# Optimization experiments

Measured on AMD Instinct MI355X. Metric: run time of the kernel, lower is better.

## Reference

```python
import jax, jax.numpy as jnp
import numpy as np

EMBED, HEADS, FF, WIN = 512, 8, 2048, 64
SIGMA, PSTRENGTH, PERIOD, THRESH = 2.0, 1.0, 100.0, 0.0


def layer_norm(x, g, b, eps=1e-5):
    mu = jnp.mean(x, axis=-1, keepdims=True)
    var = jnp.var(x, axis=-1, keepdims=True)
    return (x - mu) * jax.lax.rsqrt(var + eps) * g + b


def setup_inputs() -> dict:
    key = jax.random.key(0)
    ks = jax.random.split(key, 16)
    s = 1.0 / np.sqrt(EMBED)
    sf = 1.0 / np.sqrt(FF)
    inp = {
        "src": jax.random.normal(ks[0], (8, 2048, EMBED), dtype=jnp.float32),
        "Wq": jax.random.normal(ks[1], (EMBED, EMBED), dtype=jnp.float32) * s,
        "bq": jnp.zeros((EMBED,), jnp.float32),
        "Wk": jax.random.normal(ks[2], (EMBED, EMBED), dtype=jnp.float32) * s,
        "bk": jnp.zeros((EMBED,), jnp.float32),
        "Wv": jax.random.normal(ks[3], (EMBED, EMBED), dtype=jnp.float32) * s,
        "bv": jnp.zeros((EMBED,), jnp.float32),
        "Wo": jax.random.normal(ks[4], (EMBED, EMBED), dtype=jnp.float32) * s,
        "bo": jnp.zeros((EMBED,), jnp.float32),
        "Wg": jax.random.normal(ks[5], (EMBED, 1), dtype=jnp.float32) * s,
        "bg": jnp.zeros((1,), jnp.float32),
        "W1": jax.random.normal(ks[6], (EMBED, FF), dtype=jnp.float32) * s,
        "b1": jnp.zeros((FF,), jnp.float32),
        "W2": jax.random.normal(ks[7], (FF, EMBED), dtype=jnp.float32) * sf,
        "b2": jnp.zeros((EMBED,), jnp.float32),
        "ln1_g": jnp.ones((EMBED,), jnp.float32),
        "ln1_b": jnp.zeros((EMBED,), jnp.float32),
        "ln2_g": jnp.ones((EMBED,), jnp.float32),
        "ln2_b": jnp.zeros((EMBED,), jnp.float32),
    }
    return inp


def gated_sparse_attn(x, Wq, bq, Wk, bk, Wv, bv, Wo, bo, Wg, bg):
    B, S, D = x.shape
    H, dh = HEADS, D // HEADS
    q = (x @ Wq + bq).reshape(B, S, H, dh).transpose(0, 2, 1, 3)  # [B,H,S,dh]
    k = (x @ Wk + bk).reshape(B, S, H, dh).transpose(0, 2, 1, 3)
    v = (x @ Wv + bv).reshape(B, S, H, dh).transpose(0, 2, 1, 3)
    scores = jnp.einsum('bhqd,bhkd->bhqk', q, k) / jnp.sqrt(jnp.float32(dh))
    idx = jnp.arange(S, dtype=jnp.float32)
    dist = idx[:, None] - idx[None, :]  # [S,S]
    gauss_bias = jnp.exp(-(dist * dist) / (2.0 * SIGMA * SIGMA))
    per_bias = PSTRENGTH * jnp.cos(2.0 * jnp.pi * dist / PERIOD)
    scores = scores + gauss_bias + per_bias  # positional biases baked into scores
    local = jnp.abs(dist) <= WIN  # local-window sparsity mask
    scores = jnp.where(local, scores, jnp.float32(-1e9))
    attn = jax.nn.softmax(scores, axis=-1)
    out = jnp.einsum('bhqk,bhkd->bhqd', attn, v)
    out = out.transpose(0, 2, 1, 3).reshape(B, S, D) @ Wo + bo
    gate = jax.nn.sigmoid(x @ Wg + bg)  # [B,S,1] learned gating
    gate = jnp.where(gate > THRESH, gate, jnp.float32(0.0))
    return gate * out


def reference(src, Wq, bq, Wk, bk, Wv, bv, Wo, bo, Wg, bg, W1, b1, W2, b2, ln1_g, ln1_b, ln2_g, ln2_b):
    # dropout is identity in eval mode
    attn_out = gated_sparse_attn(src, Wq, bq, Wk, bk, Wv, bv, Wo, bo, Wg, bg)
    x = layer_norm(src + attn_out, ln1_g, ln1_b)
    ff = jax.nn.relu(x @ W1 + b1) @ W2 + b2
    return layer_norm(x + ff, ln2_g, ln2_b)
```

## Files before the change

kernel.cpp:

```cpp
#include <hip/hip_runtime.h>
#include <hip/hip_bf16.h>
#include <math.h>

#define S_LEN   2048
#define D_MOD   512
#define N_HEADS 8
#define D_HEAD  64
#define FF_DIM  2048
#define M_ROWS  16384
#define BHSD    8388608

typedef __attribute__((ext_vector_type(8))) __bf16 bf16x8;
typedef __attribute__((ext_vector_type(4))) float  f32x4;
typedef unsigned short u16;

__device__ __forceinline__ u16 f2bf(float f) {
  unsigned u = __float_as_uint(f);
  u += 0x7fffu + ((u >> 16) & 1u);
  return (u16)(u >> 16);
}
__device__ __forceinline__ float bf2f(u16 h) { return __uint_as_float(((unsigned)h) << 16); }

__device__ __forceinline__ f32x4 mfma16(bf16x8 a, bf16x8 b, f32x4 c) {
  return __builtin_amdgcn_mfma_f32_16x16x32_bf16(a, b, c, 0, 0, 0);
}

__device__ __forceinline__ void async16(void* lds, const void* g) {
  __builtin_amdgcn_global_load_lds(
      (const __attribute__((address_space(1))) unsigned int*)g,
      (__attribute__((address_space(3))) unsigned int*)lds, 16, 0, 0);
}

#define BAR()    asm volatile("s_barrier" ::: "memory")
#define WAITV(n) asm volatile("s_waitcnt vmcnt(" #n ")" ::: "memory")
#define WAITL()  asm volatile("s_waitcnt lgkmcnt(0)" ::: "memory")

__device__ __forceinline__ int swz384(int row, int bir) {
  return row * 384 + ((bir & ~127) | ((bir ^ ((row & 7) << 4)) & 127));
}

__global__ __launch_bounds__(256) void cvt_gate(const float* __restrict__ src,
                                                const float* __restrict__ Wg,
                                                const float* __restrict__ bg,
                                                u16* __restrict__ xb,
                                                float* __restrict__ gate) {
  const int wid = threadIdx.x >> 6, lane = threadIdx.x & 63;
  const size_t row = (size_t)blockIdx.x * 4 + wid;
  const float4* s = reinterpret_cast<const float4*>(src + row * D_MOD);
  const float4* w = reinterpret_cast<const float4*>(Wg);
  float4 a0 = s[lane * 2], a1 = s[lane * 2 + 1];
  float4 w0 = w[lane * 2], w1 = w[lane * 2 + 1];
  float acc = a0.x * w0.x + a0.y * w0.y + a0.z * w0.z + a0.w * w0.w +
              a1.x * w1.x + a1.y * w1.y + a1.z * w1.z + a1.w * w1.w;
#pragma unroll
  for (int m = 1; m < 64; m <<= 1) acc += __shfl_xor(acc, m);
  ushort4 h0, h1;
  h0.x = f2bf(a0.x); h0.y = f2bf(a0.y); h0.z = f2bf(a0.z); h0.w = f2bf(a0.w);
  h1.x = f2bf(a1.x); h1.y = f2bf(a1.y); h1.z = f2bf(a1.z); h1.w = f2bf(a1.w);
  ushort4* ob = reinterpret_cast<ushort4*>(xb + row * D_MOD);
  ob[lane * 2] = h0; ob[lane * 2 + 1] = h1;
  if (lane == 0) {
    float g = 1.f / (1.f + __expf(-(acc + bg[0])));
    gate[row] = g > 0.f ? g : 0.f;
  }
}

__global__ void transpose_cvt(const float* __restrict__ in, u16* __restrict__ out,
                              int K, int N) {
  __shared__ float t[32][33];
  const int n0 = blockIdx.x * 32, k0 = blockIdx.y * 32;
  const int tx = threadIdx.x, ty = threadIdx.y;
#pragma unroll
  for (int i = 0; i < 4; ++i)
    t[ty + 8 * i][tx] = in[(size_t)(k0 + ty + 8 * i) * N + n0 + tx];
  __syncthreads();
#pragma unroll
  for (int i = 0; i < 4; ++i)
    out[(size_t)(n0 + ty + 8 * i) * K + k0 + tx] = f2bf(t[tx][ty + 8 * i]);
}

__global__ __launch_bounds__(256) void ln1red_k(const float* __restrict__ src,
                                                const float* __restrict__ gate,
                                                const u16* __restrict__ p0,
                                                const u16* __restrict__ p1,
                                                const float* __restrict__ bo,
                                                const float* __restrict__ gam,
                                                const float* __restrict__ bet,
                                                u16* __restrict__ outb) {
  const int wid = threadIdx.x >> 6, lane = threadIdx.x & 63;
  const size_t row = (size_t)blockIdx.x * 4 + wid;
  const size_t base = row * D_MOD;
  const float g = gate[row];
  const float4*  sp = reinterpret_cast<const float4*>(src + base);
  const ushort4* a  = reinterpret_cast<const ushort4*>(p0 + base);
  const ushort4* c  = reinterpret_cast<const ushort4*>(p1 + base);
  const float4*  bb = reinterpret_cast<const float4*>(bo);
  float4 s0 = sp[lane * 2], s1 = sp[lane * 2 + 1];
  ushort4 a0 = a[lane * 2], a1 = a[lane * 2 + 1];
  ushort4 c0 = c[lane * 2], c1 = c[lane * 2 + 1];
  float4 d0 = bb[lane * 2], d1 = bb[lane * 2 + 1];
  float4 v0, v1;
  v0.x = s0.x + g * (bf2f(a0.x) + bf2f(c0.x) + d0.x);
  v0.y = s0.y + g * (bf2f(a0.y) + bf2f(c0.y) + d0.y);
  v0.z = s0.z + g * (bf2f(a0.z) + bf2f(c0.z) + d0.z);
  v0.w = s0.w + g * (bf2f(a0.w) + bf2f(c0.w) + d0.w);
  v1.x = s1.x + g * (bf2f(a1.x) + bf2f(c1.x) + d1.x);
  v1.y = s1.y + g * (bf2f(a1.y) + bf2f(c1.y) + d1.y);
  v1.z = s1.z + g * (bf2f(a1.z) + bf2f(c1.z) + d1.z);
  v1.w = s1.w + g * (bf2f(a1.w) + bf2f(c1.w) + d1.w);
  float s  = v0.x + v0.y + v0.z + v0.w + v1.x + v1.y + v1.z + v1.w;
  float s2 = v0.x * v0.x + v0.y * v0.y + v0.z * v0.z + v0.w * v0.w +
             v1.x * v1.x + v1.y * v1.y + v1.z * v1.z + v1.w * v1.w;
#pragma unroll
  for (int m = 1; m < 64; m <<= 1) { s += __shfl_xor(s, m); s2 += __shfl_xor(s2, m); }
  const float mu = s * (1.0f / 512.0f);
  const float var = s2 * (1.0f / 512.0f) - mu * mu;
  const float rs = 1.0f / sqrtf(var + 1e-5f);
  const float4* gp = reinterpret_cast<const float4*>(gam);
  const float4* bp = reinterpret_cast<const float4*>(bet);
  float4 g0 = gp[lane * 2], g1 = gp[lane * 2 + 1];
  float4 e0 = bp[lane * 2], e1 = bp[lane * 2 + 1];
  ushort4 h0, h1;
  h0.x = f2bf((v0.x - mu) * rs * g0.x + e0.x);  h0.y = f2bf((v0.y - mu) * rs * g0.y + e0.y);
  h0.z = f2bf((v0.z - mu) * rs * g0.z + e0.z);  h0.w = f2bf((v0.w - mu) * rs * g0.w + e0.w);
  h1.x = f2bf((v1.x - mu) * rs * g1.x + e1.x);  h1.y = f2bf((v1.y - mu) * rs * g1.y + e1.y);
  h1.z = f2bf((v1.z - mu) * rs * g1.z + e1.z);  h1.w = f2bf((v1.w - mu) * rs * g1.w + e1.w);
  ushort4* ob = reinterpret_cast<ushort4*>(outb + base);
  ob[lane * 2] = h0; ob[lane * 2 + 1] = h1;
}

__global__ __launch_bounds__(256) void ln2red_k(const u16* __restrict__ xb,
                                                const u16* __restrict__ p0,
                                                const u16* __restrict__ p1,
                                                const float* __restrict__ b2,
                                                const float* __restrict__ gam,
                                                const float* __restrict__ bet,
                                                float* __restrict__ out) {
  const int wid = threadIdx.x >> 6, lane = threadIdx.x & 63;
  const size_t row = (size_t)blockIdx.x * 4 + wid;
  const size_t base = row * D_MOD;
  const ushort4* xp = reinterpret_cast<const ushort4*>(xb + base);
  const ushort4* q0 = reinterpret_cast<const ushort4*>(p0 + base);
  const ushort4* q1 = reinterpret_cast<const ushort4*>(p1 + base);
  const float4* bb = reinterpret_cast<const float4*>(b2);
  ushort4 h0 = xp[lane * 2], h1 = xp[lane * 2 + 1];
  ushort4 a0 = q0[lane * 2], a1 = q0[lane * 2 + 1];
  ushort4 c0 = q1[lane * 2], c1 = q1[lane * 2 + 1];
  float4 d0 = bb[lane * 2], d1 = bb[lane * 2 + 1];
  float4 v0, v1;
  v0.x = bf2f(h0.x) + bf2f(a0.x) + bf2f(c0.x) + d0.x;
  v0.y = bf2f(h0.y) + bf2f(a0.y) + bf2f(c0.y) + d0.y;
  v0.z = bf2f(h0.z) + bf2f(a0.z) + bf2f(c0.z) + d0.z;
  v0.w = bf2f(h0.w) + bf2f(a0.w) + bf2f(c0.w) + d0.w;
  v1.x = bf2f(h1.x) + bf2f(a1.x) + bf2f(c1.x) + d1.x;
  v1.y = bf2f(h1.y) + bf2f(a1.y) + bf2f(c1.y) + d1.y;
  v1.z = bf2f(h1.z) + bf2f(a1.z) + bf2f(c1.z) + d1.z;
  v1.w = bf2f(h1.w) + bf2f(a1.w) + bf2f(c1.w) + d1.w;
  float s  = v0.x + v0.y + v0.z + v0.w + v1.x + v1.y + v1.z + v1.w;
  float s2 = v0.x * v0.x + v0.y * v0.y + v0.z * v0.z + v0.w * v0.w +
             v1.x * v1.x + v1.y * v1.y + v1.z * v1.z + v1.w * v1.w;
#pragma unroll
  for (int m = 1; m < 64; m <<= 1) { s += __shfl_xor(s, m); s2 += __shfl_xor(s2, m); }
  const float mu = s * (1.0f / 512.0f);
  const float var = s2 * (1.0f / 512.0f) - mu * mu;
  const float rs = 1.0f / sqrtf(var + 1e-5f);
  const float4* gp = reinterpret_cast<const float4*>(gam);
  const float4* bp = reinterpret_cast<const float4*>(bet);
  float4 g0 = gp[lane * 2], g1 = gp[lane * 2 + 1];
  float4 e0 = bp[lane * 2], e1 = bp[lane * 2 + 1];
  float4 o0, o1;
  o0.x = (v0.x - mu) * rs * g0.x + e0.x;  o0.y = (v0.y - mu) * rs * g0.y + e0.y;
  o0.z = (v0.z - mu) * rs * g0.z + e0.z;  o0.w = (v0.w - mu) * rs * g0.w + e0.w;
  o1.x = (v1.x - mu) * rs * g1.x + e1.x;  o1.y = (v1.y - mu) * rs * g1.y + e1.y;
  o1.z = (v1.z - mu) * rs * g1.z + e1.z;  o1.w = (v1.w - mu) * rs * g1.w + e1.w;
  float4* q = reinterpret_cast<float4*>(out + base);
  q[lane * 2] = o0; q[lane * 2 + 1] = o1;
}

struct EpiArgs {
  const float* b0; const float* b1; const float* b2;
  float* outf; u16* outb; u16* outb2;
};

template<int EPI, int LD, int NT, int KSLICE, int GX, int GY>
__device__ __forceinline__ void gemm256_body(const u16* __restrict__ A,
                                             const u16* __restrict__ Bt, EpiArgs e) {
  extern __shared__ char smem[];
  char* Asb = smem;
  char* Bsb = smem + 65536;
  const int tid = threadIdx.x;
  const int wid = tid >> 6, lane = tid & 63;
  const int sub = lane >> 4, lc = lane & 15;
  const int wr = wid >> 2, wcn = wid & 3;

  const int nwg = (int)(gridDim.x * gridDim.y * gridDim.z);
  const int orig = ((int)blockIdx.z * (int)gridDim.y + (int)blockIdx.y) * (int)gridDim.x + (int)blockIdx.x;
  const int cpx = nwg >> 3;
  const int wg = (orig & 7) * cpx + (orig >> 3);
  const int bx = wg % GX;
  const int by = (wg / GX) % GY;
  const int bz = wg / (GX * GY);
  const int m0 = by * 256, n0 = bx * 256;
  const int kb = KSLICE * bz;

  const u16* Ab = A + (size_t)m0 * LD;
  const u16* Bb = Bt + (size_t)n0 * LD;

  f32x4 acc[8][4];
#pragma unroll
  for (int i = 0; i < 8; ++i)
#pragma unroll
    for (int j = 0; j < 4; ++j) acc[i][j] = (f32x4){0.f, 0.f, 0.f, 0.f};

  const int lr0 = tid >> 3;
  const int sl  = tid & 7;

#define STAGE(BASE, SRC, BUF, KT)                                              \
  {                                                                            \
    const int kk_ = kb + (KT) * 64;                                            \
    _Pragma("unroll")                                                          \
    for (int r_ = 0; r_ < 4; ++r_) {                                           \
      const int lr_ = r_ * 64 + lr0;                                           \
      async16((BASE) + (BUF) * 32768 + r_ * 8192 + wid * 1024,                 \
              (SRC) + (size_t)lr_ * LD + kk_ + ((sl ^ (lr_ & 7)) << 3));       \
    }                                                                          \
  }
#define LDFRAG(BASE, ROW, KS) \
  (*reinterpret_cast<const bf16x8*>((BASE) + (ROW) * 128 + ((((KS) * 64) + sub * 16) ^ (((ROW) & 7) << 4))))

  STAGE(Bsb, Bb, 0, 0);
  STAGE(Asb, Ab, 0, 0);
  STAGE(Bsb, Bb, 1, 1);
  STAGE(Asb, Ab, 1, 1);
  WAITV(8);
  BAR();

  for (int t = 0; t < NT; ++t) {
    const int buf = t & 1;
    char* Abl = Asb + buf * 32768;
    char* Bbl = Bsb + buf * 32768;
    bf16x8 af[4][2], bfr[2][2][2];
#pragma unroll
    for (int f = 0; f < 4; ++f) {
      const int row = wr * 128 + f * 16 + lc;
#pragma unroll
      for (int ks = 0; ks < 2; ++ks) af[f][ks] = LDFRAG(Abl, row, ks);
    }
#pragma unroll
    for (int f = 0; f < 2; ++f) {
      const int row = wcn * 64 + f * 16 + lc;
#pragma unroll
      for (int ks = 0; ks < 2; ++ks) bfr[0][f][ks] = LDFRAG(Bbl, row, ks);
    }
    __builtin_amdgcn_s_setprio(1);
#pragma unroll
    for (int f = 0; f < 4; ++f)
#pragma unroll
      for (int c = 0; c < 2; ++c)
#pragma unroll
        for (int ks = 0; ks < 2; ++ks)
          acc[f][c] = mfma16(af[f][ks], bfr[0][c][ks], acc[f][c]);
    __builtin_amdgcn_s_setprio(0);
    BAR();
#pragma unroll
    for (int f = 0; f < 2; ++f) {
      const int row = wcn * 64 + 32 + f * 16 + lc;
#pragma unroll
      for (int ks = 0; ks < 2; ++ks) bfr[1][f][ks] = LDFRAG(Bbl, row, ks);
    }
    __builtin_amdgcn_s_setprio(1);
#pragma unroll
    for (int f = 0; f < 4; ++f)
#pragma unroll
      for (int c = 0; c < 2; ++c)
#pragma unroll
        for (int ks = 0; ks < 2; ++ks)
          acc[f][2 + c] = mfma16(af[f][ks], bfr[1][c][ks], acc[f][2 + c]);
    __builtin_amdgcn_s_setprio(0);
    WAITL();
    BAR();
    if (t + 2 < NT) STAGE(Bsb, Bb, buf, t + 2);
#pragma unroll
    for (int f = 0; f < 4; ++f) {
      const int row = wr * 128 + 64 + f * 16 + lc;
#pragma unroll
      for (int ks = 0; ks < 2; ++ks) af[f][ks] = LDFRAG(Abl, row, ks);
    }
    __builtin_amdgcn_s_setprio(1);
#pragma unroll
    for (int f = 0; f < 4; ++f)
#pragma unroll
      for (int c = 0; c < 2; ++c)
#pragma unroll
        for (int ks = 0; ks < 2; ++ks)
          acc[4 + f][2 + c] = mfma16(af[f][ks], bfr[1][c][ks], acc[4 + f][2 + c]);
    __builtin_amdgcn_s_setprio(0);
    WAITL();
    BAR();
    if (t + 2 < NT) STAGE(Asb, Ab, buf, t + 2);
    __builtin_amdgcn_s_setprio(1);
#pragma unroll
    for (int f = 0; f < 4; ++f)
#pragma unroll
      for (int c = 0; c < 2; ++c)
#pragma unroll
        for (int ks = 0; ks < 2; ++ks)
          acc[4 + f][c] = mfma16(af[f][ks], bfr[0][c][ks], acc[4 + f][c]);
    __builtin_amdgcn_s_setprio(0);
    if (t + 1 < NT) {
      if (t + 2 < NT) { WAITV(8); } else { WAITV(0); }
      BAR();
    }
  }
#undef STAGE
#undef LDFRAG

#pragma unroll
  for (int fr = 0; fr < 8; ++fr) {
    const int row0 = m0 + wr * 128 + fr * 16 + sub * 4;
#pragma unroll
    for (int fc = 0; fc < 4; ++fc) {
      const int col = n0 + wcn * 64 + fc * 16 + lc;
      f32x4 v = acc[fr][fc];
#pragma unroll
      for (int i = 0; i < 4; ++i) {
        const int row = row0 + i;
        const float val = v[i];
        if constexpr (EPI == 0) {
          const int which = col >> 9, nn = col & 511;
          const int hh = nn >> 6, dd = nn & 63;
          const float* bp = (which == 0) ? e.b0 : (which == 1) ? e.b1 : e.b2;
          const int bb = row >> 11, ss = row & 2047;
          e.outb[(size_t)which * BHSD + (((size_t)bb * N_HEADS + hh) * S_LEN + ss) * D_HEAD + dd]
              = f2bf(val + bp[nn]);
        } else if constexpr (EPI == 2) {
          float o = val + e.b0[col];
          e.outb[(size_t)row * FF_DIM + col] = f2bf(o > 0.f ? o : 0.f);
        } else {
          u16* dst = (bz == 0) ? e.outb : e.outb2;
          dst[(size_t)row * D_MOD + col] = f2bf(val);
        }
      }
    }
  }
}

__global__ __launch_bounds__(512, 2) void k_qkv(const u16* __restrict__ A, const u16* __restrict__ B, EpiArgs e) {
  gemm256_body<0, 512, 8, 0, 6, 64>(A, B, e);
}
__global__ __launch_bounds__(512, 2) void k_ff1(const u16* __restrict__ A, const u16* __restrict__ B, EpiArgs e) {
  gemm256_body<2, 512, 8, 0, 8, 64>(A, B, e);
}
__global__ __launch_bounds__(512, 2) void k_ff2(const u16* __restrict__ A, const u16* __restrict__ B, EpiArgs e) {
  gemm256_body<4, 2048, 16, 1024, 2, 64>(A, B, e);
}
__global__ __launch_bounds__(512, 2) void k_proj(const u16* __restrict__ A, const u16* __restrict__ B, EpiArgs e) {
  gemm256_body<4, 512, 4, 256, 2, 64>(A, B, e);
}

__global__ __launch_bounds__(256)
void attn_k(const u16* __restrict__ Q, const u16* __restrict__ Kt,
            const u16* __restrict__ V, u16* __restrict__ Oflat) {
  __shared__ __align__(16) u16 VT[64 * 192];
  __shared__ __align__(16) u16 P [64 * 192];
  __shared__ float tab[256];
  const int tid = threadIdx.x;
  const int wid = tid >> 6, lane = tid & 63;
  const int sub = lane >> 4, lc = lane & 15;
  const int qb = blockIdx.x, bh = blockIdx.y;
  const int bb = bh >> 3, hh = bh & 7;
  const int q0 = qb * 64, kstart = q0 - 64;
  const u16* Qb = Q  + (size_t)bh * S_LEN * D_HEAD;
  const u16* Kb = Kt + (size_t)bh * S_LEN * D_HEAD;
  const u16* Vb = V  + (size_t)bh * S_LEN * D_HEAD;

  if (tid < 255) {
    const int di = tid - 127;
    const float fd = (float)di;
    tab[tid] = (di >= -64 && di <= 64)
        ? __expf(-fd * fd * 0.125f) + __cosf(0.06283185307179586f * fd)
        : -1e9f;
  }

#pragma unroll
  for (int i = 0; i < 6; ++i) {
    const int c = tid + 256 * i;
    const int kk = c >> 3, dc = (c & 7) * 8;
    const int kg = kstart + kk;
    uint4 val = {0u, 0u, 0u, 0u};
    if (kg >= 0 && kg < S_LEN)
      val = *reinterpret_cast<const uint4*>(Vb + (size_t)kg * D_HEAD + dc);
    const u16* pv = reinterpret_cast<const u16*>(&val);
#pragma unroll
    for (int j = 0; j < 8; ++j)
      *reinterpret_cast<u16*>(reinterpret_cast<char*>(VT) + swz384(dc + j, kk * 2)) = pv[j];
  }

  bf16x8 qf[2];
#pragma unroll
  for (int ks = 0; ks < 2; ++ks)
    qf[ks] = *reinterpret_cast<const bf16x8*>(Qb + (size_t)(q0 + wid * 16 + lc) * D_HEAD + ks * 32 + sub * 8);

  f32x4 sc[12];
#pragma unroll
  for (int t = 0; t < 12; ++t) sc[t] = (f32x4){0.f, 0.f, 0.f, 0.f};
#pragma unroll
  for (int ks = 0; ks < 2; ++ks)
#pragma unroll
    for (int t = 0; t < 12; ++t) {
      int kg = kstart + t * 16 + lc;
      int kc = kg < 0 ? 0 : (kg > S_LEN - 1 ? S_LEN - 1 : kg);
      bf16x8 kf = *reinterpret_cast<const bf16x8*>(Kb + (size_t)kc * D_HEAD + ks * 32 + sub * 8);
      sc[t] = mfma16(qf[ks], kf, sc[t]);
    }
  __syncthreads();

  float rmax[4] = {-3e38f, -3e38f, -3e38f, -3e38f};
#pragma unroll
  for (int t = 0; t < 12; ++t) {
    const int kk = t * 16 + lc;
    const int kg = kstart + kk;
    const bool valid = (kg >= 0) && (kg < S_LEN);
#pragma unroll
    for (int r = 0; r < 4; ++r) {
      const int qrow = wid * 16 + sub * 4 + r;
      const float bias = valid ? tab[qrow - kk + 191] : -1e9f;
      const float sv = sc[t][r] * 0.125f + bias;
      sc[t][r] = sv;
      rmax[r] = fmaxf(rmax[r], sv);
    }
  }
#pragma unroll
  for (int m = 1; m < 16; m <<= 1)
#pragma unroll
    for (int r = 0; r < 4; ++r) rmax[r] = fmaxf(rmax[r], __shfl_xor(rmax[r], m));
  float rsum[4] = {0.f, 0.f, 0.f, 0.f};
#pragma unroll
  for (int t = 0; t < 12; ++t)
#pragma unroll
    for (int r = 0; r < 4; ++r) {
      const float p = __expf(sc[t][r] - rmax[r]);
      sc[t][r] = p; rsum[r] += p;
    }
#pragma unroll
  for (int m = 1; m < 16; m <<= 1)
#pragma unroll
    for (int r = 0; r < 4; ++r) rsum[r] += __shfl_xor(rsum[r], m);
  float rinv[4];
#pragma unroll
  for (int r = 0; r < 4; ++r) rinv[r] = 1.0f / rsum[r];
#pragma unroll
  for (int t = 0; t < 12; ++t)
#pragma unroll
    for (int r = 0; r < 4; ++r) {
      const int qrow = wid * 16 + sub * 4 + r;
      *reinterpret_cast<u16*>(reinterpret_cast<char*>(P) + swz384(qrow, (t * 16 + lc) * 2))
          = f2bf(sc[t][r] * rinv[r]);
    }
  __syncthreads();

  f32x4 oacc[4];
#pragma unroll
  for (int t = 0; t < 4; ++t) oacc[t] = (f32x4){0.f, 0.f, 0.f, 0.f};
  const int arow = wid * 16 + lc;
#pragma unroll
  for (int ks = 0; ks < 6; ++ks) {
    const int bir = ks * 64 + sub * 16;
    bf16x8 pa = *reinterpret_cast<const bf16x8*>(reinterpret_cast<char*>(P) + swz384(arow, bir));
#pragma unroll
    for (int t = 0; t < 4; ++t) {
      bf16x8 vb = *reinterpret_cast<const bf16x8*>(reinterpret_cast<char*>(VT) + swz384(t * 16 + lc, bir));
      oacc[t] = mfma16(pa, vb, oacc[t]);
    }
  }

  const size_t obase = ((size_t)bb * S_LEN + q0) * D_MOD + hh * D_HEAD;
#pragma unroll
  for (int t = 0; t < 4; ++t)
#pragma unroll
    for (int r = 0; r < 4; ++r) {
      const int qrow = wid * 16 + sub * 4 + r;
      Oflat[obase + (size_t)qrow * D_MOD + t * 16 + lc] = f2bf(oacc[t][r]);
    }
}

extern "C" void kernel_launch(void* const* d_in, const int* in_sizes, int n_in,
                              void* d_out, int out_size, void* d_ws, size_t ws_size,
                              hipStream_t stream) {
  (void)in_sizes; (void)n_in; (void)out_size; (void)ws_size;
  const float* src  = (const float*)d_in[0];
  const float* Wq   = (const float*)d_in[1];
  const float* bq   = (const float*)d_in[2];
  const float* Wk   = (const float*)d_in[3];
  const float* bk   = (const float*)d_in[4];
  const float* Wv   = (const float*)d_in[5];
  const float* bv   = (const float*)d_in[6];
  const float* Wo   = (const float*)d_in[7];
  const float* bo   = (const float*)d_in[8];
  const float* Wg   = (const float*)d_in[9];
  const float* bg   = (const float*)d_in[10];
  const float* W1   = (const float*)d_in[11];
  const float* b1   = (const float*)d_in[12];
  const float* W2   = (const float*)d_in[13];
  const float* b2   = (const float*)d_in[14];
  const float* ln1g = (const float*)d_in[15];
  const float* ln1b = (const float*)d_in[16];
  const float* ln2g = (const float*)d_in[17];
  const float* ln2b = (const float*)d_in[18];
  float* out = (float*)d_out;

  char* ws = (char*)d_ws;
  u16*   WqkvT  = (u16*)  (ws + 0);
  u16*   WoT    = (u16*)  (ws + 1572864);
  u16*   W1T    = (u16*)  (ws + 2097152);
  u16*   W2T    = (u16*)  (ws + 4194304);
  float* gatef  = (float*)(ws + 6291456);
  u16*   Xbf    = (u16*)  (ws + 6356992);
  u16*   QKVbf  = (u16*)  (ws + 23134208);
  u16*   attnfl = (u16*)  (ws + 73465856);
  u16*   pr0    = (u16*)  (ws + 90243072);
  u16*   pr1    = (u16*)  (ws + 107020288);
  u16*   xbf2   = (u16*)  (ws + 123797504);
  u16*   hbuf   = Xbf;
  u16*   pf0    = pr0;
  u16*   pf1    = pr1;

  (void)hipFuncSetAttribute((const void*)k_qkv,  hipFuncAttributeMaxDynamicSharedMemorySize, 131072);
  (void)hipFuncSetAttribute((const void*)k_ff1,  hipFuncAttributeMaxDynamicSharedMemorySize, 131072);
  (void)hipFuncSetAttribute((const void*)k_ff2,  hipFuncAttributeMaxDynamicSharedMemorySize, 131072);
  (void)hipFuncSetAttribute((const void*)k_proj, hipFuncAttributeMaxDynamicSharedMemorySize, 131072);

  dim3 tb(32, 8);
  cvt_gate<<<4096, 256, 0, stream>>>(src, Wg, bg, Xbf, gatef);
  transpose_cvt<<<dim3(16, 16), tb, 0, stream>>>(Wq, WqkvT,             512, 512);
  transpose_cvt<<<dim3(16, 16), tb, 0, stream>>>(Wk, WqkvT + 512 * 512, 512, 512);
  transpose_cvt<<<dim3(16, 16), tb, 0, stream>>>(Wv, WqkvT + 2 * 512 * 512, 512, 512);
  transpose_cvt<<<dim3(16, 16), tb, 0, stream>>>(Wo, WoT, 512, 512);
  transpose_cvt<<<dim3(64, 16), tb, 0, stream>>>(W1, W1T, 512, 2048);
  transpose_cvt<<<dim3(16, 64), tb, 0, stream>>>(W2, W2T, 2048, 512);

  EpiArgs e1{bq, bk, bv, nullptr, QKVbf, nullptr};
  k_qkv<<<dim3(6, 64, 1), 512, 131072, stream>>>(Xbf, WqkvT, e1);

  attn_k<<<dim3(32, 64), 256, 0, stream>>>(QKVbf, QKVbf + BHSD, QKVbf + 2 * BHSD, attnfl);

  EpiArgs e2{nullptr, nullptr, nullptr, nullptr, pr0, pr1};
  k_proj<<<dim3(2, 64, 2), 512, 131072, stream>>>(attnfl, WoT, e2);

  ln1red_k<<<4096, 256, 0, stream>>>(src, gatef, pr0, pr1, bo, ln1g, ln1b, xbf2);

  EpiArgs e3{b1, nullptr, nullptr, nullptr, hbuf, nullptr};
  k_ff1<<<dim3(8, 64, 1), 512, 131072, stream>>>(xbf2, W1T, e3);

  EpiArgs e4{nullptr, nullptr, nullptr, nullptr, pf0, pf1};
  k_ff2<<<dim3(2, 64, 2), 512, 131072, stream>>>(hbuf, W2T, e4);

  ln2red_k<<<4096, 256, 0, stream>>>(xbf2, pf0, pf1, b2, ln2g, ln2b, out);
}
```

Before: 222.6 us.

## Keep attention probabilities in registers via transposed MFMA and shuffles; bf16 residual in LN1

The attention kernel swaps the MFMA operand order so each lane holds one query row's scores. Softmax then needs only two cross-lane shuffles, and the normalized probabilities are packed with v_cvt_pk_bf16_f32 and rearranged by lane shuffles straight into the PV MFMA operand. This drops the P LDS round trip and one barrier. The output is staged through a small swizzled LDS buffer so each lane writes 16-byte coalesced global stores. Separately, the LN1 residual now reads the bf16 copy of src instead of fp32, which halves that read but loses precision in the residual path.

```diff
diff --git a/kernel.cpp b/kernel.cpp
--- a/kernel.cpp
+++ b/kernel.cpp
@@ -23,6 +23,12 @@
 
 __device__ __forceinline__ f32x4 mfma16(bf16x8 a, bf16x8 b, f32x4 c) {
   return __builtin_amdgcn_mfma_f32_16x16x32_bf16(a, b, c, 0, 0, 0);
+}
+
+__device__ __forceinline__ unsigned pkbf(float a, float b) {
+  unsigned r;
+  asm("v_cvt_pk_bf16_f32 %0, %1, %2" : "=v"(r) : "v"(a), "v"(b));
+  return r;
 }
 
 __device__ __forceinline__ void async16(void* lds, const void* g) {
@@ -79,7 +85,7 @@
     out[(size_t)(n0 + ty + 8 * i) * K + k0 + tx] = f2bf(t[tx][ty + 8 * i]);
 }
 
-__global__ __launch_bounds__(256) void ln1red_k(const float* __restrict__ src,
+__global__ __launch_bounds__(256) void ln1red_k(const u16* __restrict__ xb,
                                                 const float* __restrict__ gate,
                                                 const u16* __restrict__ p0,
                                                 const u16* __restrict__ p1,
@@ -91,23 +97,23 @@
   const size_t row = (size_t)blockIdx.x * 4 + wid;
   const size_t base = row * D_MOD;
   const float g = gate[row];
-  const float4*  sp = reinterpret_cast<const float4*>(src + base);
+  const ushort4* sp = reinterpret_cast<const ushort4*>(xb + base);
   const ushort4* a  = reinterpret_cast<const ushort4*>(p0 + base);
   const ushort4* c  = reinterpret_cast<const ushort4*>(p1 + base);
   const float4*  bb = reinterpret_cast<const float4*>(bo);
-  float4 s0 = sp[lane * 2], s1 = sp[lane * 2 + 1];
+  ushort4 s0 = sp[lane * 2], s1 = sp[lane * 2 + 1];
   ushort4 a0 = a[lane * 2], a1 = a[lane * 2 + 1];
   ushort4 c0 = c[lane * 2], c1 = c[lane * 2 + 1];
   float4 d0 = bb[lane * 2], d1 = bb[lane * 2 + 1];
   float4 v0, v1;
-  v0.x = s0.x + g * (bf2f(a0.x) + bf2f(c0.x) + d0.x);
-  v0.y = s0.y + g * (bf2f(a0.y) + bf2f(c0.y) + d0.y);
-  v0.z = s0.z + g * (bf2f(a0.z) + bf2f(c0.z) + d0.z);
-  v0.w = s0.w + g * (bf2f(a0.w) + bf2f(c0.w) + d0.w);
-  v1.x = s1.x + g * (bf2f(a1.x) + bf2f(c1.x) + d1.x);
-  v1.y = s1.y + g * (bf2f(a1.y) + bf2f(c1.y) + d1.y);
-  v1.z = s1.z + g * (bf2f(a1.z) + bf2f(c1.z) + d1.z);
-  v1.w = s1.w + g * (bf2f(a1.w) + bf2f(c1.w) + d1.w);
+  v0.x = bf2f(s0.x) + g * (bf2f(a0.x) + bf2f(c0.x) + d0.x);
+  v0.y = bf2f(s0.y) + g * (bf2f(a0.y) + bf2f(c0.y) + d0.y);
+  v0.z = bf2f(s0.z) + g * (bf2f(a0.z) + bf2f(c0.z) + d0.z);
+  v0.w = bf2f(s0.w) + g * (bf2f(a0.w) + bf2f(c0.w) + d0.w);
+  v1.x = bf2f(s1.x) + g * (bf2f(a1.x) + bf2f(c1.x) + d1.x);
+  v1.y = bf2f(s1.y) + g * (bf2f(a1.y) + bf2f(c1.y) + d1.y);
+  v1.z = bf2f(s1.z) + g * (bf2f(a1.z) + bf2f(c1.z) + d1.z);
+  v1.w = bf2f(s1.w) + g * (bf2f(a1.w) + bf2f(c1.w) + d1.w);
   float s  = v0.x + v0.y + v0.z + v0.w + v1.x + v1.y + v1.z + v1.w;
   float s2 = v0.x * v0.x + v0.y * v0.y + v0.z * v0.z + v0.w * v0.w +
              v1.x * v1.x + v1.y * v1.y + v1.z * v1.z + v1.w * v1.w;
@@ -362,7 +368,7 @@
 void attn_k(const u16* __restrict__ Q, const u16* __restrict__ Kt,
             const u16* __restrict__ V, u16* __restrict__ Oflat) {
   __shared__ __align__(16) u16 VT[64 * 192];
-  __shared__ __align__(16) u16 P [64 * 192];
+  __shared__ __align__(16) char Ob[8192];
   __shared__ float tab[256];
   const int tid = threadIdx.x;
   const int wid = tid >> 6, lane = tid & 63;
@@ -411,77 +417,88 @@
       int kg = kstart + t * 16 + lc;
       int kc = kg < 0 ? 0 : (kg > S_LEN - 1 ? S_LEN - 1 : kg);
       bf16x8 kf = *reinterpret_cast<const bf16x8*>(Kb + (size_t)kc * D_HEAD + ks * 32 + sub * 8);
-      sc[t] = mfma16(qf[ks], kf, sc[t]);
+      sc[t] = mfma16(kf, qf[ks], sc[t]);
     }
   __syncthreads();
 
-  float rmax[4] = {-3e38f, -3e38f, -3e38f, -3e38f};
-#pragma unroll
-  for (int t = 0; t < 12; ++t) {
-    const int kk = t * 16 + lc;
-    const int kg = kstart + kk;
-    const bool valid = (kg >= 0) && (kg < S_LEN);
+  const int qrow = wid * 16 + lc;
+  float m = -3e38f;
+#pragma unroll
+  for (int t = 0; t < 12; ++t)
 #pragma unroll
     for (int r = 0; r < 4; ++r) {
-      const int qrow = wid * 16 + sub * 4 + r;
+      const int kk = t * 16 + 4 * sub + r;
+      const int kg = kstart + kk;
+      const bool valid = (kg >= 0) && (kg < S_LEN);
       const float bias = valid ? tab[qrow - kk + 191] : -1e9f;
       const float sv = sc[t][r] * 0.125f + bias;
       sc[t][r] = sv;
-      rmax[r] = fmaxf(rmax[r], sv);
-    }
-  }
-#pragma unroll
-  for (int m = 1; m < 16; m <<= 1)
-#pragma unroll
-    for (int r = 0; r < 4; ++r) rmax[r] = fmaxf(rmax[r], __shfl_xor(rmax[r], m));
-  float rsum[4] = {0.f, 0.f, 0.f, 0.f};
+      m = fmaxf(m, sv);
+    }
+  m = fmaxf(m, __shfl_xor(m, 16));
+  m = fmaxf(m, __shfl_xor(m, 32));
+  float sum = 0.f;
 #pragma unroll
   for (int t = 0; t < 12; ++t)
 #pragma unroll
     for (int r = 0; r < 4; ++r) {
-      const float p = __expf(sc[t][r] - rmax[r]);
-      sc[t][r] = p; rsum[r] += p;
-    }
-#pragma unroll
-  for (int m = 1; m < 16; m <<= 1)
-#pragma unroll
-    for (int r = 0; r < 4; ++r) rsum[r] += __shfl_xor(rsum[r], m);
-  float rinv[4];
-#pragma unroll
-  for (int r = 0; r < 4; ++r) rinv[r] = 1.0f / rsum[r];
-#pragma unroll
-  for (int t = 0; t < 12; ++t)
-#pragma unroll
-    for (int r = 0; r < 4; ++r) {
-      const int qrow = wid * 16 + sub * 4 + r;
-      *reinterpret_cast<u16*>(reinterpret_cast<char*>(P) + swz384(qrow, (t * 16 + lc) * 2))
-          = f2bf(sc[t][r] * rinv[r]);
-    }
+      const float p = __expf(sc[t][r] - m);
+      sc[t][r] = p; sum += p;
+    }
+  sum += __shfl_xor(sum, 16);
+  sum += __shfl_xor(sum, 32);
+  const float rinv = 1.0f / sum;
+
+  f32x4 oacc[4];
+#pragma unroll
+  for (int t = 0; t < 4; ++t) oacc[t] = (f32x4){0.f, 0.f, 0.f, 0.f};
+  const int srcA = lc + ((sub & 1) << 5);
+#pragma unroll
+  for (int s = 0; s < 6; ++s) {
+    const unsigned d00 = pkbf(sc[2 * s][0] * rinv, sc[2 * s][1] * rinv);
+    const unsigned d01 = pkbf(sc[2 * s][2] * rinv, sc[2 * s][3] * rinv);
+    const unsigned d10 = pkbf(sc[2 * s + 1][0] * rinv, sc[2 * s + 1][1] * rinv);
+    const unsigned d11 = pkbf(sc[2 * s + 1][2] * rinv, sc[2 * s + 1][3] * rinv);
+    const unsigned uA0 = (unsigned)__shfl((int)d00, srcA);
+    const unsigned uA1 = (unsigned)__shfl((int)d01, srcA);
+    const unsigned uB0 = (unsigned)__shfl((int)d00, srcA + 16);
+    const unsigned uB1 = (unsigned)__shfl((int)d01, srcA + 16);
+    const unsigned vA0 = (unsigned)__shfl((int)d10, srcA);
+    const unsigned vA1 = (unsigned)__shfl((int)d11, srcA);
+    const unsigned vB0 = (unsigned)__shfl((int)d10, srcA + 16);
+    const unsigned vB1 = (unsigned)__shfl((int)d11, srcA + 16);
+    const bool lo = (sub < 2);
+    uint4 wv;
+    wv.x = lo ? uA0 : vA0;  wv.y = lo ? uA1 : vA1;
+    wv.z = lo ? uB0 : vB0;  wv.w = lo ? uB1 : vB1;
+    const bf16x8 pf = __builtin_bit_cast(bf16x8, wv);
+#pragma unroll
+    for (int t = 0; t < 4; ++t) {
+      bf16x8 vf = *reinterpret_cast<const bf16x8*>(
+          reinterpret_cast<char*>(VT) + swz384(16 * t + lc, 64 * s + 16 * sub));
+      oacc[t] = mfma16(vf, pf, oacc[t]);
+    }
+  }
+
+  char* obw = Ob + wid * 2048 + lc * 128;
+#pragma unroll
+  for (int t = 0; t < 4; ++t) {
+    const unsigned o01 = pkbf(oacc[t][0], oacc[t][1]);
+    const unsigned o23 = pkbf(oacc[t][2], oacc[t][3]);
+    const int b0 = (32 * t + 8 * sub) ^ ((lc & 7) << 4);
+    *reinterpret_cast<unsigned*>(obw + b0) = o01;
+    *reinterpret_cast<unsigned*>(obw + b0 + 4) = o23;
+  }
   __syncthreads();
-
-  f32x4 oacc[4];
-#pragma unroll
-  for (int t = 0; t < 4; ++t) oacc[t] = (f32x4){0.f, 0.f, 0.f, 0.f};
-  const int arow = wid * 16 + lc;
-#pragma unroll
-  for (int ks = 0; ks < 6; ++ks) {
-    const int bir = ks * 64 + sub * 16;
-    bf16x8 pa = *reinterpret_cast<const bf16x8*>(reinterpret_cast<char*>(P) + swz384(arow, bir));
-#pragma unroll
-    for (int t = 0; t < 4; ++t) {
-      bf16x8 vb = *reinterpret_cast<const bf16x8*>(reinterpret_cast<char*>(VT) + swz384(t * 16 + lc, bir));
-      oacc[t] = mfma16(pa, vb, oacc[t]);
-    }
-  }
-
-  const size_t obase = ((size_t)bb * S_LEN + q0) * D_MOD + hh * D_HEAD;
-#pragma unroll
-  for (int t = 0; t < 4; ++t)
-#pragma unroll
-    for (int r = 0; r < 4; ++r) {
-      const int qrow = wid * 16 + sub * 4 + r;
-      Oflat[obase + (size_t)qrow * D_MOD + t * 16 + lc] = f2bf(oacc[t][r]);
-    }
+  const int qp = lane >> 2;
+  const int cb = (lane & 3) * 32;
+  const size_t orow = (size_t)bb * S_LEN + q0 + wid * 16 + qp;
+#pragma unroll
+  for (int h = 0; h < 2; ++h) {
+    const int rb = (cb + h * 16) ^ ((qp & 7) << 4);
+    uint4 v = *reinterpret_cast<const uint4*>(Ob + wid * 2048 + qp * 128 + rb);
+    *reinterpret_cast<uint4*>(Oflat + orow * D_MOD + hh * D_HEAD + (lane & 3) * 16 + h * 8) = v;
+  }
 }
 
 extern "C" void kernel_launch(void* const* d_in, const int* in_sizes, int n_in,
@@ -547,7 +564,7 @@
   EpiArgs e2{nullptr, nullptr, nullptr, nullptr, pr0, pr1};
   k_proj<<<dim3(2, 64, 2), 512, 131072, stream>>>(attnfl, WoT, e2);
 
-  ln1red_k<<<4096, 256, 0, stream>>>(src, gatef, pr0, pr1, bo, ln1g, ln1b, xbf2);
+  ln1red_k<<<4096, 256, 0, stream>>>(Xbf, gatef, pr0, pr1, bo, ln1g, ln1b, xbf2);
 
   EpiArgs e3{b1, nullptr, nullptr, nullptr, hbuf, nullptr};
   k_ff1<<<dim3(8, 64, 1), 512, 131072, stream>>>(xbf2, W1T, e3);
```

Measured after the change: 227.0 us. No clear change (+2.0%).

## Pre-transpose V into global layout and read bf16 residual in LN1

Applied to the files above, without the earlier changes.

Adds a separate kernel that transposes V per head into a [D_HEAD, S] global buffer. The attention kernel can then fill its swizzled VT shared tile with 16-byte async copies instead of scattering 2-byte stores. The LN1 kernel also reads the residual from the bf16 copy of src instead of the fp32 original, which halves that read but lowers the residual to bf16 precision. The trade-off is an extra launch and roughly 33 MB of extra global traffic for the transposed V, and the clamped sb index at sequence edges may load shifted data where the old code zero-filled.

```diff
diff --git a/kernel.cpp b/kernel.cpp
--- a/kernel.cpp
+++ b/kernel.cpp
@@ -79,7 +79,43 @@
     out[(size_t)(n0 + ty + 8 * i) * K + k0 + tx] = f2bf(t[tx][ty + 8 * i]);
 }
 
-__global__ __launch_bounds__(256) void ln1red_k(const float* __restrict__ src,
+__global__ __launch_bounds__(256) void vtr_k(const u16* __restrict__ V,
+                                             u16* __restrict__ VT) {
+  __shared__ __align__(16) u16 T[64 * 64];
+  const int tid = threadIdx.x;
+  const int wid = tid >> 6, lane = tid & 63;
+  const int bh = blockIdx.y;
+  const int s0 = blockIdx.x * 64;
+  const u16* Vb = V + ((size_t)bh * S_LEN + s0) * D_HEAD;
+#pragma unroll
+  for (int r = 0; r < 2; ++r) {
+    const int c = r * 256 + tid;
+    const int s = c >> 3;
+    const int blk = (c & 7) ^ ((s >> 3) & 7);
+    async16((char*)T + (r * 4 + wid) * 1024, Vb + (size_t)s * D_HEAD + blk * 8);
+  }
+  __syncthreads();
+  u16* VTb = VT + (size_t)bh * D_HEAD * S_LEN;
+#pragma unroll
+  for (int r = 0; r < 2; ++r) {
+    const int d  = (r * 4 + wid) * 8 + (lane >> 3);
+    const int s8 = lane & 7;
+    ushort4 w0, w1;
+    u16 tmp[8];
+#pragma unroll
+    for (int j = 0; j < 8; ++j) {
+      const int s = s8 * 8 + j;
+      tmp[j] = *reinterpret_cast<const u16*>(
+          (const char*)T + s * 128 + ((2 * d) ^ (((s >> 3) & 7) << 4)));
+    }
+    w0.x = tmp[0]; w0.y = tmp[1]; w0.z = tmp[2]; w0.w = tmp[3];
+    w1.x = tmp[4]; w1.y = tmp[5]; w1.z = tmp[6]; w1.w = tmp[7];
+    ushort4* dst = reinterpret_cast<ushort4*>(VTb + (size_t)d * S_LEN + s0 + s8 * 8);
+    dst[0] = w0; dst[1] = w1;
+  }
+}
+
+__global__ __launch_bounds__(256) void ln1red_k(const u16* __restrict__ xb,
                                                 const float* __restrict__ gate,
                                                 const u16* __restrict__ p0,
                                                 const u16* __restrict__ p1,
@@ -91,23 +127,23 @@
   const size_t row = (size_t)blockIdx.x * 4 + wid;
   const size_t base = row * D_MOD;
   const float g = gate[row];
-  const float4*  sp = reinterpret_cast<const float4*>(src + base);
+  const ushort4* sp = reinterpret_cast<const ushort4*>(xb + base);
   const ushort4* a  = reinterpret_cast<const ushort4*>(p0 + base);
   const ushort4* c  = reinterpret_cast<const ushort4*>(p1 + base);
   const float4*  bb = reinterpret_cast<const float4*>(bo);
-  float4 s0 = sp[lane * 2], s1 = sp[lane * 2 + 1];
+  ushort4 s0 = sp[lane * 2], s1 = sp[lane * 2 + 1];
   ushort4 a0 = a[lane * 2], a1 = a[lane * 2 + 1];
   ushort4 c0 = c[lane * 2], c1 = c[lane * 2 + 1];
   float4 d0 = bb[lane * 2], d1 = bb[lane * 2 + 1];
   float4 v0, v1;
-  v0.x = s0.x + g * (bf2f(a0.x) + bf2f(c0.x) + d0.x);
-  v0.y = s0.y + g * (bf2f(a0.y) + bf2f(c0.y) + d0.y);
-  v0.z = s0.z + g * (bf2f(a0.z) + bf2f(c0.z) + d0.z);
-  v0.w = s0.w + g * (bf2f(a0.w) + bf2f(c0.w) + d0.w);
-  v1.x = s1.x + g * (bf2f(a1.x) + bf2f(c1.x) + d1.x);
-  v1.y = s1.y + g * (bf2f(a1.y) + bf2f(c1.y) + d1.y);
-  v1.z = s1.z + g * (bf2f(a1.z) + bf2f(c1.z) + d1.z);
-  v1.w = s1.w + g * (bf2f(a1.w) + bf2f(c1.w) + d1.w);
+  v0.x = bf2f(s0.x) + g * (bf2f(a0.x) + bf2f(c0.x) + d0.x);
+  v0.y = bf2f(s0.y) + g * (bf2f(a0.y) + bf2f(c0.y) + d0.y);
+  v0.z = bf2f(s0.z) + g * (bf2f(a0.z) + bf2f(c0.z) + d0.z);
+  v0.w = bf2f(s0.w) + g * (bf2f(a0.w) + bf2f(c0.w) + d0.w);
+  v1.x = bf2f(s1.x) + g * (bf2f(a1.x) + bf2f(c1.x) + d1.x);
+  v1.y = bf2f(s1.y) + g * (bf2f(a1.y) + bf2f(c1.y) + d1.y);
+  v1.z = bf2f(s1.z) + g * (bf2f(a1.z) + bf2f(c1.z) + d1.z);
+  v1.w = bf2f(s1.w) + g * (bf2f(a1.w) + bf2f(c1.w) + d1.w);
   float s  = v0.x + v0.y + v0.z + v0.w + v1.x + v1.y + v1.z + v1.w;
   float s2 = v0.x * v0.x + v0.y * v0.y + v0.z * v0.z + v0.w * v0.w +
              v1.x * v1.x + v1.y * v1.y + v1.z * v1.z + v1.w * v1.w;
@@ -360,7 +396,7 @@
 
 __global__ __launch_bounds__(256)
 void attn_k(const u16* __restrict__ Q, const u16* __restrict__ Kt,
-            const u16* __restrict__ V, u16* __restrict__ Oflat) {
+            const u16* __restrict__ VTg, u16* __restrict__ Oflat) {
   __shared__ __align__(16) u16 VT[64 * 192];
   __shared__ __align__(16) u16 P [64 * 192];
   __shared__ float tab[256];
@@ -372,7 +408,18 @@
   const int q0 = qb * 64, kstart = q0 - 64;
   const u16* Qb = Q  + (size_t)bh * S_LEN * D_HEAD;
   const u16* Kb = Kt + (size_t)bh * S_LEN * D_HEAD;
-  const u16* Vb = V  + (size_t)bh * S_LEN * D_HEAD;
+  const u16* Vtb = VTg + (size_t)bh * D_HEAD * S_LEN;
+
+#pragma unroll
+  for (int it = 0; it < 6; ++it) {
+    const int c = (wid * 6 + it) * 64 + lane;
+    const int row = c / 24;
+    const int bir = (c % 24) * 16;
+    const int swz = (bir & ~127) | ((bir ^ ((row & 7) << 4)) & 127);
+    int sb = kstart + (swz >> 1);
+    sb = sb < 0 ? 0 : (sb > S_LEN - 8 ? S_LEN - 8 : sb);
+    async16((char*)VT + (wid * 6 + it) * 1024, Vtb + (size_t)row * S_LEN + sb);
+  }
 
   if (tid < 255) {
     const int di = tid - 127;
@@ -380,20 +427,6 @@
     tab[tid] = (di >= -64 && di <= 64)
         ? __expf(-fd * fd * 0.125f) + __cosf(0.06283185307179586f * fd)
         : -1e9f;
-  }
-
-#pragma unroll
-  for (int i = 0; i < 6; ++i) {
-    const int c = tid + 256 * i;
-    const int kk = c >> 3, dc = (c & 7) * 8;
-    const int kg = kstart + kk;
-    uint4 val = {0u, 0u, 0u, 0u};
-    if (kg >= 0 && kg < S_LEN)
-      val = *reinterpret_cast<const uint4*>(Vb + (size_t)kg * D_HEAD + dc);
-    const u16* pv = reinterpret_cast<const u16*>(&val);
-#pragma unroll
-    for (int j = 0; j < 8; ++j)
-      *reinterpret_cast<u16*>(reinterpret_cast<char*>(VT) + swz384(dc + j, kk * 2)) = pv[j];
   }
 
   bf16x8 qf[2];
@@ -521,6 +554,7 @@
   u16*   pr0    = (u16*)  (ws + 90243072);
   u16*   pr1    = (u16*)  (ws + 107020288);
   u16*   xbf2   = (u16*)  (ws + 123797504);
+  u16*   VTg    = (u16*)  (ws + 140574720);
   u16*   hbuf   = Xbf;
   u16*   pf0    = pr0;
   u16*   pf1    = pr1;
@@ -542,12 +576,14 @@
   EpiArgs e1{bq, bk, bv, nullptr, QKVbf, nullptr};
   k_qkv<<<dim3(6, 64, 1), 512, 131072, stream>>>(Xbf, WqkvT, e1);
 
-  attn_k<<<dim3(32, 64), 256, 0, stream>>>(QKVbf, QKVbf + BHSD, QKVbf + 2 * BHSD, attnfl);
+  vtr_k<<<dim3(32, 64), 256, 0, stream>>>(QKVbf + 2 * BHSD, VTg);
+
+  attn_k<<<dim3(32, 64), 256, 0, stream>>>(QKVbf, QKVbf + BHSD, VTg, attnfl);
 
   EpiArgs e2{nullptr, nullptr, nullptr, nullptr, pr0, pr1};
   k_proj<<<dim3(2, 64, 2), 512, 131072, stream>>>(attnfl, WoT, e2);
 
-  ln1red_k<<<4096, 256, 0, stream>>>(src, gatef, pr0, pr1, bo, ln1g, ln1b, xbf2);
+  ln1red_k<<<4096, 256, 0, stream>>>(Xbf, gatef, pr0, pr1, bo, ln1g, ln1b, xbf2);
 
   EpiArgs e3{b1, nullptr, nullptr, nullptr, hbuf, nullptr};
   k_ff1<<<dim3(8, 64, 1), 512, 131072, stream>>>(xbf2, W1T, e3);
```

After: 223.4 us. Within noise of the previous version (+0.4%).
